# Optimization experiments

Hardware: AMD Instinct MI355X
Metric: run time of the kernel (lower is better)

The kernel has to match this reference:

```python
import jax, jax.numpy as jnp
import numpy as np

N_FEAT = 64      # number of continuous features
N_BINS = 255     # bin edges per feature (EBM default) -> 256 score slots incl. OOV
N_PAIRS = 32     # interaction terms
BATCH = 262144


def _bin_indices(edges, x):
    """TF Discretization (searchsorted right) + IntegerLookup(vocab=range(B), OOV->0).
    edges: [N, B] sorted per row; x: [batch, N] -> int32 [batch, N] in [0, B]."""
    idx = jax.vmap(lambda e, col: jnp.searchsorted(e, col, side='right'),
                   in_axes=(0, 1), out_axes=1)(edges, x)  # [batch, N], values 0..B
    B = edges.shape[1]
    # IntegerLookup: value v in {0..B-1} -> v+1 ; value B (not in vocab) -> OOV index 0
    return jnp.where(idx < B, idx + 1, 0)


def setup_inputs() -> dict:
    key = jax.random.key(0)
    ks = jax.random.split(key, 6)
    x = jax.random.normal(ks[0], (BATCH, N_FEAT), dtype=jnp.float32)
    edges = jnp.sort(jax.random.normal(ks[1], (N_FEAT, N_BINS), dtype=jnp.float32), axis=1)
    pair_edges = jnp.sort(jax.random.normal(ks[2], (N_FEAT, N_BINS), dtype=jnp.float32), axis=1)
    w = jax.random.normal(ks[3], (N_FEAT, N_BINS + 1), dtype=jnp.float32) * 0.1
    tables = jax.random.normal(ks[4], (N_PAIRS, N_BINS + 1, N_BINS + 1), dtype=jnp.float32) * 0.1
    pairs = jax.random.randint(ks[5], (N_PAIRS, 2), 0, N_FEAT, dtype=jnp.int32)
    bias = jnp.zeros((1,), dtype=jnp.float32)
    return {"x": x, "edges": edges, "w": w, "pair_edges": pair_edges,
            "pairs": pairs, "tables": tables, "bias": bias}


def reference(x, edges, w, pair_edges, pairs, tables, bias):
    # --- per-feature main effects: one_hot(idx) @ Dense(1) == gather w[f, idx] ---
    idx = _bin_indices(edges, x)                                  # [batch, N]
    feat = w[jnp.arange(N_FEAT)[None, :], idx]                    # [batch, N]
    # --- pairwise interactions: gather_nd on [L, R] lookup tables ---
    pidx = _bin_indices(pair_edges, x)                            # [batch, N]
    li = pidx[:, pairs[:, 0]]                                     # [batch, P]
    ri = pidx[:, pairs[:, 1]]                                     # [batch, P]
    inter = tables[jnp.arange(N_PAIRS)[None, :], li, ri]          # [batch, P]
    # --- BiasLayer: reduce_sum(concat, axis=1) + bias, then sigmoid ---
    logits = jnp.sum(feat, axis=1) + jnp.sum(inter, axis=1) + bias[0]
    return jax.nn.sigmoid(logits)                                  # [batch]
```

## Files before the change

### kernel.cpp

```cpp
#include <hip/hip_runtime.h>
#include <hip/hip_fp16.h>

#define NBINS 255
#define NPAIRS 32
#define BIGF 3.0e38f


__global__ void ebm_prep(const float* __restrict__ edges,
                         const float* __restrict__ pair_edges,
                         const float* __restrict__ w,
                         float* __restrict__ ws) {
    int tid = blockIdx.x * blockDim.x + threadIdx.x;
    int f = tid >> 8, j = tid & 255;
    float* E  = ws;
    float* PE = ws + 16384;
    float* ME = ws + 32768;
    float* MP = ws + 36864;
    float* CU = ws + 40960;
    float* CP = ws + 41984;
    __half* W = (__half*)(ws + 43008);
    E[tid]  = (j < NBINS) ? edges[f * NBINS + j]      : BIGF;
    PE[tid] = (j < NBINS) ? pair_edges[f * NBINS + j] : BIGF;
    int src = (j < 255) ? j + 1 : 0;
    W[tid]  = __float2half(w[f * 256 + src]);
    if (j < 64) {
        int idx = 4 * j + 3;
        ME[f * 64 + j] = (idx < NBINS) ? edges[f * NBINS + idx]      : BIGF;
        MP[f * 64 + j] = (idx < NBINS) ? pair_edges[f * NBINS + idx] : BIGF;
    }
    if (j < 16) {
        CU[f * 16 + j] = (j < 15) ? edges[f * NBINS + 16 * j + 15]      : BIGF;
        CP[f * 16 + j] = (j < 15) ? pair_edges[f * NBINS + 16 * j + 15] : BIGF;
    }
}

__global__ void ebm_prep_tables(const float* __restrict__ tables,
                                unsigned short* __restrict__ o) {
    int i = blockIdx.x * blockDim.x + threadIdx.x;
    int b = i & 255, a = (i >> 8) & 255, p = i >> 16;
    int ra = (a < 255) ? a + 1 : 0;
    int rb = (b < 255) ? b + 1 : 0;
    o[i] = __half_as_ushort(__float2half(tables[(p << 16) + (ra << 8) + rb]));
}

__global__ __launch_bounds__(512, 8) void ebm_bins(
    const float* __restrict__ x,
    const int*   __restrict__ pairs,
    float* ws) {

    __shared__ float  sE[4096];
    __shared__ float  sPE[4096];
    __shared__ float4 sME[256];
    __shared__ float4 sMP[256];

    int tid = threadIdx.x;
    int q  = blockIdx.x & 3;
    int row = (blockIdx.x >> 2) * 512 + tid;
    int f0 = q * 16;

    const float4* w4 = (const float4*)ws;
    {
        float4* dE = (float4*)sE;
        float4* dP = (float4*)sPE;
        dE[tid]       = w4[f0 * 64 + tid];
        dE[tid + 512] = w4[f0 * 64 + tid + 512];
        dP[tid]       = w4[4096 + f0 * 64 + tid];
        dP[tid + 512] = w4[4096 + f0 * 64 + tid + 512];
        if (tid < 256) {
            sME[tid] = w4[8192 + f0 * 16 + tid];
            sMP[tid] = w4[9216 + f0 * 16 + tid];
        }
    }

    unsigned long long mask = 0;
#pragma unroll 1
    for (int k = 0; k < 2 * NPAIRS; ++k) mask |= 1ull << pairs[k];

    __syncthreads();

    const float*  CU = ws + 40960;
    const float*  CP = ws + 41984;
    const __half* Wg = (const __half*)(ws + 43008);
    const float4* sE4 = (const float4*)sE;
    const float4* sP4 = (const float4*)sPE;
    const float4* x4 = (const float4*)x + (size_t)row * 16;

    float acc = 0.f;
    unsigned pwq[4];

#pragma unroll
    for (int g = 0; g < 4; ++g) {
        float4 xg = x4[q * 4 + g];
        float xf[4] = {xg.x, xg.y, xg.z, xg.w};

        int t[4];
#pragma unroll
        for (int j = 0; j < 4; ++j) {
            const float* cu = CU + (f0 + 4 * g + j) * 16;
            int tt = 0;
#pragma unroll
            for (int k = 0; k < 15; ++k) tt += (xf[j] >= cu[k]);
            t[j] = tt;
        }
        float4 mu[4];
#pragma unroll
        for (int j = 0; j < 4; ++j) mu[j] = sME[(4 * g + j) * 16 + t[j]];
        int lo[4];
        float4 fu[4];
#pragma unroll
        for (int j = 0; j < 4; ++j) {
            int m = (xf[j] >= mu[j].x) + (xf[j] >= mu[j].y) + (xf[j] >= mu[j].z);
            lo[j] = 4 * t[j] + m;
            fu[j] = sE4[(4 * g + j) * 64 + lo[j]];
        }
#pragma unroll
        for (int j = 0; j < 4; ++j) {
            int c = 4 * lo[j] + (xf[j] >= fu[j].x) + (xf[j] >= fu[j].y) +
                    (xf[j] >= fu[j].z) + (xf[j] >= fu[j].w);
            acc += __half2float(Wg[(f0 + 4 * g + j) * 256 + c]);
        }

        unsigned pword = 0;
#pragma unroll
        for (int j = 0; j < 4; ++j) {
            int f = f0 + 4 * g + j;
            if ((mask >> f) & 1) {
                const float* cp = CP + f * 16;
                int tt = 0;
#pragma unroll
                for (int k = 0; k < 15; ++k) tt += (xf[j] >= cp[k]);
                float4 mp = sMP[(4 * g + j) * 16 + tt];
                int m = (xf[j] >= mp.x) + (xf[j] >= mp.y) + (xf[j] >= mp.z);
                int l2 = 4 * tt + m;
                float4 fp = sP4[(4 * g + j) * 64 + l2];
                int c2 = 4 * l2 + (xf[j] >= fp.x) + (xf[j] >= fp.y) +
                         (xf[j] >= fp.z) + (xf[j] >= fp.w);
                pword |= (unsigned)c2 << (8 * j);
            }
        }
        pwq[g] = pword;
    }

    float* P = ws + 51200;
    P[q * 262144 + row] = acc;
    unsigned* PW = (unsigned*)(ws + 1099776);
#pragma unroll
    for (int g = 0; g < 4; ++g) PW[(q * 4 + g) * 262144 + row] = pwq[g];
}

__global__ __launch_bounds__(256, 8) void ebm_pairs(
    const int*   __restrict__ pairs,
    const float* __restrict__ tables_f32,
    const float* __restrict__ bias,
    const float* __restrict__ ws,
    const __half* __restrict__ T16,
    int useT16,
    float* __restrict__ out) {

    __shared__ unsigned char sB[256 * 68];
    int tid = threadIdx.x;
    int row = blockIdx.x * 256 + tid;

    const float* P = ws + 51200;
    float acc = bias[0] + P[row] + P[262144 + row] + P[524288 + row] + P[786432 + row];

    const unsigned* PW = (const unsigned*)(ws + 1099776);
    unsigned* myw = (unsigned*)(sB + tid * 68);
#pragma unroll
    for (int k = 0; k < 16; ++k) myw[k] = PW[k * 262144 + row];

    const unsigned char* me = sB + tid * 68;
    if (useT16) {
#pragma unroll
        for (int p = 0; p < NPAIRS; ++p) {
            int a = pairs[2 * p], b = pairs[2 * p + 1];
            int li = me[a], ri = me[b];
            acc += __half2float(T16[(p << 16) + (li << 8) + ri]);
        }
    } else {
#pragma unroll
        for (int p = 0; p < NPAIRS; ++p) {
            int a = pairs[2 * p], b = pairs[2 * p + 1];
            int li = me[a], ri = me[b];
            int lb = (li < 255) ? li + 1 : 0, rb = (ri < 255) ? ri + 1 : 0;
            acc += tables_f32[(p << 16) + (lb << 8) + rb];
        }
    }
    out[row] = 1.0f / (1.0f + __expf(-acc));
}

__device__ __forceinline__ unsigned pick16(const unsigned* pw, int s) {
    unsigned v01 = (s & 1) ? pw[1]  : pw[0];
    unsigned v23 = (s & 1) ? pw[3]  : pw[2];
    unsigned v45 = (s & 1) ? pw[5]  : pw[4];
    unsigned v67 = (s & 1) ? pw[7]  : pw[6];
    unsigned v89 = (s & 1) ? pw[9]  : pw[8];
    unsigned vab = (s & 1) ? pw[11] : pw[10];
    unsigned vcd = (s & 1) ? pw[13] : pw[12];
    unsigned vef = (s & 1) ? pw[15] : pw[14];
    unsigned w0 = (s & 2) ? v23 : v01;
    unsigned w1 = (s & 2) ? v67 : v45;
    unsigned w2 = (s & 2) ? vab : v89;
    unsigned w3 = (s & 2) ? vef : vcd;
    unsigned u0 = (s & 4) ? w1 : w0;
    unsigned u1 = (s & 4) ? w3 : w2;
    return (s & 8) ? u1 : u0;
}

__global__ __launch_bounds__(1024) void ebm_mono(
    const float* __restrict__ x,
    const int*   __restrict__ pairs,
    const float* __restrict__ tables_f32,
    const float* __restrict__ bias,
    const float* __restrict__ ws,
    const __half* __restrict__ T16,
    int useT16,
    float*       __restrict__ out) {

    __shared__ float  sE[16384];
    __shared__ float  sPE[16384];
    __shared__ float4 sME[1024];
    __shared__ float4 sMP[1024];

    int tid = threadIdx.x;
    {
        const float4* w4 = (const float4*)ws;
        float4* dE = (float4*)sE;
        float4* dP = (float4*)sPE;
        for (int i = tid; i < 4096; i += 1024) {
            dE[i] = w4[i];
            dP[i] = w4[4096 + i];
        }
        if (tid < 1024) {
            sME[tid] = w4[8192 + tid];
            sMP[tid] = w4[9216 + tid];
        }
    }
    const float*  CU = ws + 40960;
    const float*  CP = ws + 41984;
    const __half* Wg = (const __half*)(ws + 43008);
    float bias0 = bias[0];

    __syncthreads();

    int row = blockIdx.x * 1024 + tid;
    const float4* x4 = (const float4*)x + (size_t)row * 16;
    const float4* sE4 = (const float4*)sE;
    const float4* sP4 = (const float4*)sPE;

    float acc = 0.f;
    unsigned pw[16];

    float4 xg = x4[0];
#pragma unroll
    for (int g = 0; g < 16; ++g) {
        float4 xnext = xg;
        if (g < 15) xnext = x4[g + 1];
        float xf[4] = {xg.x, xg.y, xg.z, xg.w};
        int t[4];
#pragma unroll
        for (int j = 0; j < 4; ++j) {
            const float* cu = CU + (4 * g + j) * 16;
            int tt = 0;
#pragma unroll
            for (int k = 0; k < 15; ++k) tt += (xf[j] >= cu[k]);
            t[j] = tt;
        }
        int t2[4];
#pragma unroll
        for (int j = 0; j < 4; ++j) {
            const float* cp = CP + (4 * g + j) * 16;
            int tt = 0;
#pragma unroll
            for (int k = 0; k < 15; ++k) tt += (xf[j] >= cp[k]);
            t2[j] = tt;
        }
        float4 mu[4], mp[4];
#pragma unroll
        for (int j = 0; j < 4; ++j) mu[j] = sME[(4 * g + j) * 16 + t[j]];
#pragma unroll
        for (int j = 0; j < 4; ++j) mp[j] = sMP[(4 * g + j) * 16 + t2[j]];
        int lo[4], lo2[4];
        float4 fu[4], fp[4];
#pragma unroll
        for (int j = 0; j < 4; ++j) {
            int m = (xf[j] >= mu[j].x) + (xf[j] >= mu[j].y) + (xf[j] >= mu[j].z);
            lo[j] = 4 * t[j] + m;
            fu[j] = sE4[(4 * g + j) * 64 + lo[j]];
        }
#pragma unroll
        for (int j = 0; j < 4; ++j) {
            int m = (xf[j] >= mp[j].x) + (xf[j] >= mp[j].y) + (xf[j] >= mp[j].z);
            lo2[j] = 4 * t2[j] + m;
            fp[j] = sP4[(4 * g + j) * 64 + lo2[j]];
        }
#pragma unroll
        for (int j = 0; j < 4; ++j) {
            int c = 4 * lo[j] + (xf[j] >= fu[j].x) + (xf[j] >= fu[j].y) +
                    (xf[j] >= fu[j].z) + (xf[j] >= fu[j].w);
            acc += __half2float(Wg[(4 * g + j) * 256 + c]);
        }
        unsigned pword = 0;
#pragma unroll
        for (int j = 0; j < 4; ++j) {
            int c2 = 4 * lo2[j] + (xf[j] >= fp[j].x) + (xf[j] >= fp[j].y) +
                     (xf[j] >= fp[j].z) + (xf[j] >= fp[j].w);
            pword |= (unsigned)c2 << (8 * j);
        }
        pw[g] = pword;
        xg = xnext;
    }

    if (useT16) {
#pragma unroll
        for (int p = 0; p < NPAIRS; ++p) {
            int a = pairs[2 * p], b = pairs[2 * p + 1];
            unsigned wa = pick16(pw, a >> 2);
            unsigned wb = pick16(pw, b >> 2);
            int li = (wa >> ((a & 3) * 8)) & 255;
            int ri = (wb >> ((b & 3) * 8)) & 255;
            acc += __half2float(T16[(p << 16) + (li << 8) + ri]);
        }
    } else {
#pragma unroll
        for (int p = 0; p < NPAIRS; ++p) {
            int a = pairs[2 * p], b = pairs[2 * p + 1];
            unsigned wa = pick16(pw, a >> 2);
            unsigned wb = pick16(pw, b >> 2);
            int li = (wa >> ((a & 3) * 8)) & 255;
            int ri = (wb >> ((b & 3) * 8)) & 255;
            int lb = (li < 255) ? li + 1 : 0;
            int rb = (ri < 255) ? ri + 1 : 0;
            acc += tables_f32[(p << 16) + (lb << 8) + rb];
        }
    }
    out[row] = 1.0f / (1.0f + __expf(-(acc + bias0)));
}

extern "C" void kernel_launch(void* const* d_in, const int* in_sizes, int n_in,
                              void* d_out, int out_size, void* d_ws, size_t ws_size,
                              hipStream_t stream) {
    const float* x          = (const float*)d_in[0];
    const float* edges      = (const float*)d_in[1];
    const float* w          = (const float*)d_in[2];
    const float* pair_edges = (const float*)d_in[3];
    const int*   pairs      = (const int*)d_in[4];
    const float* tables     = (const float*)d_in[5];
    const float* bias       = (const float*)d_in[6];
    float* out = (float*)d_out;
    float* ws  = (float*)d_ws;

    ebm_prep<<<64, 256, 0, stream>>>(edges, pair_edges, w, ws);

    if (ws_size >= (size_t)21176320) {
        int useT16 = (ws_size >= (size_t)25370624) ? 1 : 0;
        __half* T16 = (__half*)((char*)d_ws + 21176320);
        if (useT16) {
            ebm_prep_tables<<<2048, 1024, 0, stream>>>(tables, (unsigned short*)T16);
        }
        ebm_bins<<<2048, 512, 0, stream>>>(x, pairs, ws);
        ebm_pairs<<<1024, 256, 0, stream>>>(pairs, tables, bias, ws, T16, useT16, out);
    } else {
        int useT16 = (ws_size >= (size_t)4399104) ? 1 : 0;
        __half* T16 = (__half*)((char*)d_ws + 204800);
        if (useT16) {
            ebm_prep_tables<<<2048, 1024, 0, stream>>>(tables, (unsigned short*)T16);
        }
        ebm_mono<<<256, 1024, 0, stream>>>(x, pairs, tables, bias, ws, T16, useT16, out);
    }
}
```

Baseline: 209.0 us.

## Fuse prep kernels and split work into unary and pair-fused passes

Merges edge prep and the table fp16 conversion into one launch. It replaces the 4-way feature-split bins kernel plus the separate pairs kernel with two full-row kernels: one for main effects, and one that recomputes the pair bins and does the table gathers directly. This drops the large intermediate pair-index buffer write and read and one kernel launch. In exchange, x is read twice, and each block uses 80KB of shared memory with 1024 threads, which limits occupancy.

```diff
diff --git a/kernel.cpp b/kernel.cpp
--- a/kernel.cpp
+++ b/kernel.cpp
@@ -6,12 +6,10 @@
 #define BIGF 3.0e38f
 
 
-__global__ void ebm_prep(const float* __restrict__ edges,
-                         const float* __restrict__ pair_edges,
-                         const float* __restrict__ w,
-                         float* __restrict__ ws) {
-    int tid = blockIdx.x * blockDim.x + threadIdx.x;
-    int f = tid >> 8, j = tid & 255;
+__device__ __forceinline__ void prep_edge_elem(int i,
+        const float* __restrict__ edges, const float* __restrict__ pair_edges,
+        const float* __restrict__ w, float* __restrict__ ws) {
+    int f = i >> 8, j = i & 255;
     float* E  = ws;
     float* PE = ws + 16384;
     float* ME = ws + 32768;
@@ -19,10 +17,10 @@
     float* CU = ws + 40960;
     float* CP = ws + 41984;
     __half* W = (__half*)(ws + 43008);
-    E[tid]  = (j < NBINS) ? edges[f * NBINS + j]      : BIGF;
-    PE[tid] = (j < NBINS) ? pair_edges[f * NBINS + j] : BIGF;
+    E[i]  = (j < NBINS) ? edges[f * NBINS + j]      : BIGF;
+    PE[i] = (j < NBINS) ? pair_edges[f * NBINS + j] : BIGF;
     int src = (j < 255) ? j + 1 : 0;
-    W[tid]  = __float2half(w[f * 256 + src]);
+    W[i]  = __float2half(w[f * 256 + src]);
     if (j < 64) {
         int idx = 4 * j + 3;
         ME[f * 64 + j] = (idx < NBINS) ? edges[f * NBINS + idx]      : BIGF;
@@ -32,6 +30,28 @@
         CU[f * 16 + j] = (j < 15) ? edges[f * NBINS + 16 * j + 15]      : BIGF;
         CP[f * 16 + j] = (j < 15) ? pair_edges[f * NBINS + 16 * j + 15] : BIGF;
     }
+}
+
+__global__ void ebm_prep_all(const float* __restrict__ edges,
+                             const float* __restrict__ pair_edges,
+                             const float* __restrict__ w,
+                             const float* __restrict__ tables,
+                             float* __restrict__ ws,
+                             unsigned short* __restrict__ T16o) {
+    int i = blockIdx.x * blockDim.x + threadIdx.x;
+    int b = i & 255, a = (i >> 8) & 255, p = i >> 16;
+    int ra = (a < 255) ? a + 1 : 0;
+    int rb = (b < 255) ? b + 1 : 0;
+    T16o[i] = __half_as_ushort(__float2half(tables[(p << 16) + (ra << 8) + rb]));
+    if (i < 16384) prep_edge_elem(i, edges, pair_edges, w, ws);
+}
+
+__global__ void ebm_prep(const float* __restrict__ edges,
+                         const float* __restrict__ pair_edges,
+                         const float* __restrict__ w,
+                         float* __restrict__ ws) {
+    int i = blockIdx.x * blockDim.x + threadIdx.x;
+    prep_edge_elem(i, edges, pair_edges, w, ws);
 }
 
 __global__ void ebm_prep_tables(const float* __restrict__ tables,
@@ -43,60 +63,39 @@
     o[i] = __half_as_ushort(__float2half(tables[(p << 16) + (ra << 8) + rb]));
 }
 
-__global__ __launch_bounds__(512, 8) void ebm_bins(
+__global__ __launch_bounds__(1024, 8) void ebm_unary(
     const float* __restrict__ x,
-    const int*   __restrict__ pairs,
-    float* ws) {
-
-    __shared__ float  sE[4096];
-    __shared__ float  sPE[4096];
-    __shared__ float4 sME[256];
-    __shared__ float4 sMP[256];
+    float* __restrict__ ws) {
+
+    __shared__ __align__(16) char smem[81920];
+    float*  sE  = (float*)smem;
+    float4* sME = (float4*)(smem + 65536);
 
     int tid = threadIdx.x;
-    int q  = blockIdx.x & 3;
-    int row = (blockIdx.x >> 2) * 512 + tid;
-    int f0 = q * 16;
-
-    const float4* w4 = (const float4*)ws;
     {
+        const float4* w4 = (const float4*)ws;
         float4* dE = (float4*)sE;
-        float4* dP = (float4*)sPE;
-        dE[tid]       = w4[f0 * 64 + tid];
-        dE[tid + 512] = w4[f0 * 64 + tid + 512];
-        dP[tid]       = w4[4096 + f0 * 64 + tid];
-        dP[tid + 512] = w4[4096 + f0 * 64 + tid + 512];
-        if (tid < 256) {
-            sME[tid] = w4[8192 + f0 * 16 + tid];
-            sMP[tid] = w4[9216 + f0 * 16 + tid];
-        }
-    }
-
-    unsigned long long mask = 0;
-#pragma unroll 1
-    for (int k = 0; k < 2 * NPAIRS; ++k) mask |= 1ull << pairs[k];
-
+#pragma unroll
+        for (int k = 0; k < 4; ++k) dE[tid + 1024 * k] = w4[tid + 1024 * k];
+        sME[tid] = w4[8192 + tid];
+    }
     __syncthreads();
 
     const float*  CU = ws + 40960;
-    const float*  CP = ws + 41984;
     const __half* Wg = (const __half*)(ws + 43008);
+    int row = blockIdx.x * 1024 + tid;
+    const float4* x4  = (const float4*)x + (size_t)row * 16;
     const float4* sE4 = (const float4*)sE;
-    const float4* sP4 = (const float4*)sPE;
-    const float4* x4 = (const float4*)x + (size_t)row * 16;
 
     float acc = 0.f;
-    unsigned pwq[4];
-
-#pragma unroll
-    for (int g = 0; g < 4; ++g) {
-        float4 xg = x4[q * 4 + g];
+#pragma unroll
+    for (int g = 0; g < 16; ++g) {
+        float4 xg = x4[g];
         float xf[4] = {xg.x, xg.y, xg.z, xg.w};
-
         int t[4];
 #pragma unroll
         for (int j = 0; j < 4; ++j) {
-            const float* cu = CU + (f0 + 4 * g + j) * 16;
+            const float* cu = CU + (4 * g + j) * 16;
             int tt = 0;
 #pragma unroll
             for (int k = 0; k < 15; ++k) tt += (xf[j] >= cu[k]);
@@ -117,38 +116,14 @@
         for (int j = 0; j < 4; ++j) {
             int c = 4 * lo[j] + (xf[j] >= fu[j].x) + (xf[j] >= fu[j].y) +
                     (xf[j] >= fu[j].z) + (xf[j] >= fu[j].w);
-            acc += __half2float(Wg[(f0 + 4 * g + j) * 256 + c]);
-        }
-
-        unsigned pword = 0;
-#pragma unroll
-        for (int j = 0; j < 4; ++j) {
-            int f = f0 + 4 * g + j;
-            if ((mask >> f) & 1) {
-                const float* cp = CP + f * 16;
-                int tt = 0;
-#pragma unroll
-                for (int k = 0; k < 15; ++k) tt += (xf[j] >= cp[k]);
-                float4 mp = sMP[(4 * g + j) * 16 + tt];
-                int m = (xf[j] >= mp.x) + (xf[j] >= mp.y) + (xf[j] >= mp.z);
-                int l2 = 4 * tt + m;
-                float4 fp = sP4[(4 * g + j) * 64 + l2];
-                int c2 = 4 * l2 + (xf[j] >= fp.x) + (xf[j] >= fp.y) +
-                         (xf[j] >= fp.z) + (xf[j] >= fp.w);
-                pword |= (unsigned)c2 << (8 * j);
-            }
-        }
-        pwq[g] = pword;
-    }
-
-    float* P = ws + 51200;
-    P[q * 262144 + row] = acc;
-    unsigned* PW = (unsigned*)(ws + 1099776);
-#pragma unroll
-    for (int g = 0; g < 4; ++g) PW[(q * 4 + g) * 262144 + row] = pwq[g];
-}
-
-__global__ __launch_bounds__(256, 8) void ebm_pairs(
+            acc += __half2float(Wg[(4 * g + j) * 256 + c]);
+        }
+    }
+    ws[51200 + row] = acc;
+}
+
+__global__ __launch_bounds__(1024, 8) void ebm_pairf(
+    const float* __restrict__ x,
     const int*   __restrict__ pairs,
     const float* __restrict__ tables_f32,
     const float* __restrict__ bias,
@@ -157,19 +132,62 @@
     int useT16,
     float* __restrict__ out) {
 
-    __shared__ unsigned char sB[256 * 68];
+    __shared__ __align__(16) char smem[81920];
+    float*  sPE = (float*)smem;
+    float4* sMP = (float4*)(smem + 65536);
+
     int tid = threadIdx.x;
-    int row = blockIdx.x * 256 + tid;
-
-    const float* P = ws + 51200;
-    float acc = bias[0] + P[row] + P[262144 + row] + P[524288 + row] + P[786432 + row];
-
-    const unsigned* PW = (const unsigned*)(ws + 1099776);
-    unsigned* myw = (unsigned*)(sB + tid * 68);
-#pragma unroll
-    for (int k = 0; k < 16; ++k) myw[k] = PW[k * 262144 + row];
-
-    const unsigned char* me = sB + tid * 68;
+    {
+        const float4* w4 = (const float4*)ws;
+        float4* dP = (float4*)sPE;
+#pragma unroll
+        for (int k = 0; k < 4; ++k) dP[tid + 1024 * k] = w4[4096 + tid + 1024 * k];
+        sMP[tid] = w4[9216 + tid];
+    }
+    unsigned long long mask = 0;
+#pragma unroll 1
+    for (int k = 0; k < 2 * NPAIRS; ++k) mask |= 1ull << pairs[k];
+    __syncthreads();
+
+    const float* CP = ws + 41984;
+    int row = blockIdx.x * 1024 + tid;
+    const float4* x4  = (const float4*)x + (size_t)row * 16;
+    const float4* sP4 = (const float4*)sPE;
+
+    unsigned pw[16];
+#pragma unroll
+    for (int g = 0; g < 16; ++g) {
+        float4 xg = x4[g];
+        float xf[4] = {xg.x, xg.y, xg.z, xg.w};
+        unsigned pword = 0;
+#pragma unroll
+        for (int j = 0; j < 4; ++j) {
+            int f = 4 * g + j;
+            if ((mask >> f) & 1) {
+                const float* cp = CP + f * 16;
+                int tt = 0;
+#pragma unroll
+                for (int k = 0; k < 15; ++k) tt += (xf[j] >= cp[k]);
+                float4 mp = sMP[f * 16 + tt];
+                int m = (xf[j] >= mp.x) + (xf[j] >= mp.y) + (xf[j] >= mp.z);
+                int l2 = 4 * tt + m;
+                float4 fp = sP4[f * 64 + l2];
+                int c2 = 4 * l2 + (xf[j] >= fp.x) + (xf[j] >= fp.y) +
+                         (xf[j] >= fp.z) + (xf[j] >= fp.w);
+                pword |= (unsigned)c2 << (8 * j);
+            }
+        }
+        pw[g] = pword;
+    }
+
+    __syncthreads();
+    unsigned* park = (unsigned*)smem;
+#pragma unroll
+    for (int k = 0; k < 16; ++k) park[tid * 17 + k] = pw[k];
+    __syncthreads();
+
+    const unsigned char* me = (const unsigned char*)smem + tid * 68;
+    float acc = bias[0] + ws[51200 + row];
     if (useT16) {
 #pragma unroll
         for (int p = 0; p < NPAIRS; ++p) {
@@ -231,16 +249,13 @@
             dE[i] = w4[i];
             dP[i] = w4[4096 + i];
         }
-        if (tid < 1024) {
-            sME[tid] = w4[8192 + tid];
-            sMP[tid] = w4[9216 + tid];
-        }
+        sME[tid] = w4[8192 + tid];
+        sMP[tid] = w4[9216 + tid];
     }
     const float*  CU = ws + 40960;
     const float*  CP = ws + 41984;
     const __half* Wg = (const __half*)(ws + 43008);
     float bias0 = bias[0];
-
     __syncthreads();
 
     int row = blockIdx.x * 1024 + tid;
@@ -250,14 +265,11 @@
 
     float acc = 0.f;
     unsigned pw[16];
-
-    float4 xg = x4[0];
 #pragma unroll
     for (int g = 0; g < 16; ++g) {
-        float4 xnext = xg;
-        if (g < 15) xnext = x4[g + 1];
+        float4 xg = x4[g];
         float xf[4] = {xg.x, xg.y, xg.z, xg.w};
-        int t[4];
+        int t[4], t2[4];
 #pragma unroll
         for (int j = 0; j < 4; ++j) {
             const float* cu = CU + (4 * g + j) * 16;
@@ -266,7 +278,6 @@
             for (int k = 0; k < 15; ++k) tt += (xf[j] >= cu[k]);
             t[j] = tt;
         }
-        int t2[4];
 #pragma unroll
         for (int j = 0; j < 4; ++j) {
             const float* cp = CP + (4 * g + j) * 16;
@@ -308,7 +319,6 @@
             pword |= (unsigned)c2 << (8 * j);
         }
         pw[g] = pword;
-        xg = xnext;
     }
 
     if (useT16) {
@@ -350,19 +360,16 @@
     float* out = (float*)d_out;
     float* ws  = (float*)d_ws;
 
-    ebm_prep<<<64, 256, 0, stream>>>(edges, pair_edges, w, ws);
-
-    if (ws_size >= (size_t)21176320) {
-        int useT16 = (ws_size >= (size_t)25370624) ? 1 : 0;
-        __half* T16 = (__half*)((char*)d_ws + 21176320);
-        if (useT16) {
-            ebm_prep_tables<<<2048, 1024, 0, stream>>>(tables, (unsigned short*)T16);
-        }
-        ebm_bins<<<2048, 512, 0, stream>>>(x, pairs, ws);
-        ebm_pairs<<<1024, 256, 0, stream>>>(pairs, tables, bias, ws, T16, useT16, out);
+    if (ws_size >= (size_t)5447680) {
+        __half* T16 = (__half*)((char*)d_ws + 1253376);
+        ebm_prep_all<<<2048, 1024, 0, stream>>>(edges, pair_edges, w, tables,
+                                                ws, (unsigned short*)T16);
+        ebm_unary<<<256, 1024, 0, stream>>>(x, ws);
+        ebm_pairf<<<256, 1024, 0, stream>>>(x, pairs, tables, bias, ws, T16, 1, out);
     } else {
         int useT16 = (ws_size >= (size_t)4399104) ? 1 : 0;
         __half* T16 = (__half*)((char*)d_ws + 204800);
+        ebm_prep<<<64, 256, 0, stream>>>(edges, pair_edges, w, ws);
         if (useT16) {
             ebm_prep_tables<<<2048, 1024, 0, stream>>>(tables, (unsigned short*)T16);
         }
```

Result: slower. 218.2 us (+4.4%).
